# Optimization experiments

Hardware: AMD Instinct MI355X
Metric: run time of the kernel (lower is better)

Reference implementation:

```python
import jax, jax.numpy as jnp
import numpy as np

B, V, F, H, W = 8, 5023, 9976, 512, 512
L = 5  # lights


def setup_inputs() -> dict:
    key = jax.random.key(0)
    ks = jax.random.split(key, 7)
    return {
        "vertices": jax.random.normal(ks[0], (B, V, 3), jnp.float32),
        "transformed_vertices": jax.random.normal(ks[1], (B, V, 3), jnp.float32),
        "lights": jax.random.normal(ks[2], (B, L, 6), jnp.float32),
        "images": jax.random.uniform(ks[3], (B, 3, H, W), jnp.float32),
        "bary": jax.random.uniform(ks[4], (B, H, W, 3), jnp.float32) + 1e-3,
        "faces": jax.random.randint(ks[5], (F, 3), 0, V),
        "pix_to_face": jax.random.randint(ks[6], (B, H, W), 0, F + 1),  # ==F -> background
    }


def _face_vertices(verts, faces):
    # verts [B,V,3], faces [F,3] -> [B,F,3,3]  (gather)
    return verts[:, faces]


def _vertex_normals(verts, faces):
    # gather face verts, per-face cross products, scatter-add back to vertices
    fv = verts[:, faces]                       # [B,F,3,3]
    v0, v1, v2 = fv[:, :, 0], fv[:, :, 1], fv[:, :, 2]
    n = jnp.zeros_like(verts)
    n = n.at[:, faces[:, 1]].add(jnp.cross(v2 - v1, v0 - v1))
    n = n.at[:, faces[:, 2]].add(jnp.cross(v0 - v2, v1 - v2))
    n = n.at[:, faces[:, 0]].add(jnp.cross(v1 - v0, v2 - v0))
    return n / jnp.maximum(jnp.linalg.norm(n, axis=-1, keepdims=True), 1e-6)


def _add_directionlight(normals, lights):
    # normals [B,N,3], lights [B,L,6] -> shading [B,N,3]
    d = lights[:, :, :3]
    d = d / jnp.maximum(jnp.linalg.norm(d, axis=-1, keepdims=True), 1e-12)
    ndl = jnp.clip(jnp.einsum("bnc,blc->bln", normals, d), 0.0, 1.0)  # [B,L,N]
    return jnp.mean(ndl[..., None] * lights[:, :, None, 3:], axis=1)


def reference(vertices, transformed_vertices, lights, images, bary, faces, pix_to_face):
    sg = jax.lax.stop_gradient
    b, nv, _ = vertices.shape
    nf = faces.shape[0]
    h, w = pix_to_face.shape[1], pix_to_face.shape[2]

    tv = transformed_vertices.at[:, :, 2].add(10.0)

    fverts = _face_vertices(vertices, faces)                 # [B,F,3,3]
    normals = _vertex_normals(vertices, faces)               # [B,V,3]
    fnorm = _face_vertices(normals, faces)                   # [B,F,3,3]
    tnorm = _vertex_normals(tv, faces)
    tfnorm = _face_vertices(tnorm, faces)

    colors = jnp.full((b, nf, 3, 3), 180.0 / 255.0, vertices.dtype)  # face_colors buffer
    uv = jnp.zeros((b, nf, 3, 3), vertices.dtype)                    # face_uvcoords (unused downstream)
    # attribute channels: [0:3]=albedo [3:6]=tfnorm [6:9]=verts [9:12]=fnorm [12:15]=uv
    attrs = jnp.concatenate([colors, sg(tfnorm), sg(fverts), fnorm, uv], axis=-1)  # [B,F,3,15]

    # --- rasterizer interpolation stage ---
    p2f = pix_to_face.reshape(b, -1)                         # [B,HW]
    valid = (p2f < nf).astype(vertices.dtype)[..., None]     # [B,HW,1] alpha channel
    fidx = jnp.minimum(p2f, nf - 1)
    pa = jax.vmap(lambda a, i: a[i])(attrs, fidx)            # [B,HW,3,15]
    bw = bary.reshape(b, -1, 3)
    bw = bw / jnp.sum(bw, axis=-1, keepdims=True)
    interp = jnp.einsum("bpk,bpkc->bpc", bw, pa)             # [B,HW,15]

    albedo = interp[..., 0:3]
    tnormal_map = sg(interp[..., 3:6])
    pos_mask = (tnormal_map[..., 2:3] < 0.15).astype(vertices.dtype)
    normal_images = sg(interp[..., 9:12])
    alpha = sg(valid) * pos_mask                             # [B,HW,1]

    shading = _add_directionlight(normal_images, lights)     # [B,HW,3]
    shaded = albedo * shading

    imgs = images.transpose(0, 2, 3, 1).reshape(b, -1, 3)
    out = shaded * alpha + imgs * (1.0 - alpha)              # [B,HW,3]
    return out.reshape(b, h, w, 3).transpose(0, 3, 1, 2)     # [B,3,H,W]
```

## Files before the change

### kernel.cpp

```cpp
#include <hip/hip_runtime.h>

namespace {

constexpr int kB = 8;
constexpr int kV = 5023;
constexpr int kF = 9976;
constexpr int kH = 512;
constexpr int kW = 512;
constexpr int kL = 5;
constexpr int kHW = kH * kW;
constexpr int kQ = kHW / 4;
constexpr int kCap = 32;

__device__ __forceinline__ void cross3(float ax, float ay, float az,
                                       float bx, float by, float bz,
                                       float& cx, float& cy, float& cz) {
  cx = ay * bz - az * by;
  cy = az * bx - ax * bz;
  cz = ax * by - ay * bx;
}

__global__ void init_kernel(int* __restrict__ cnt,
                            const float* __restrict__ lights,
                            float* __restrict__ ldir) {
  int idx = blockIdx.x * blockDim.x + threadIdx.x;
  for (int i = idx; i < kV; i += gridDim.x * blockDim.x) cnt[i] = 0;
  if (idx < kB * kL) {
    float dx = lights[idx * 6 + 0];
    float dy = lights[idx * 6 + 1];
    float dz = lights[idx * 6 + 2];
    float inv = 1.0f / fmaxf(sqrtf(dx * dx + dy * dy + dz * dz), 1e-12f);
    ldir[idx * 6 + 0] = dx * inv;
    ldir[idx * 6 + 1] = dy * inv;
    ldir[idx * 6 + 2] = dz * inv;
    ldir[idx * 6 + 3] = lights[idx * 6 + 3];
    ldir[idx * 6 + 4] = lights[idx * 6 + 4];
    ldir[idx * 6 + 5] = lights[idx * 6 + 5];
  }
}

__global__ void prep_kernel(const float* __restrict__ verts,
                            const float* __restrict__ tverts,
                            const int* __restrict__ faces,
                            int* __restrict__ cnt,
                            int* __restrict__ adj,
                            float4* __restrict__ fn) {
  int idx = blockIdx.x * blockDim.x + threadIdx.x;
  if (idx < kF) {
    int f = idx;
#pragma unroll
    for (int c = 0; c < 3; ++c) {
      int v = faces[f * 3 + c];
      int slot = atomicAdd(&cnt[v], 1);
      if (slot < kCap) adj[v * kCap + slot] = f;
    }
    return;
  }
  idx -= kF;
  if (idx >= kB * kF) return;
  int b = idx / kF;
  int f = idx - b * kF;
  int i0 = faces[f * 3 + 0];
  int i1 = faces[f * 3 + 1];
  int i2 = faces[f * 3 + 2];

  float nx, ny, nz, tx, ty, tz;
  {
    const float* vb = verts + (size_t)b * kV * 3;
    float v0x = vb[i0 * 3 + 0], v0y = vb[i0 * 3 + 1], v0z = vb[i0 * 3 + 2];
    float v1x = vb[i1 * 3 + 0], v1y = vb[i1 * 3 + 1], v1z = vb[i1 * 3 + 2];
    float v2x = vb[i2 * 3 + 0], v2y = vb[i2 * 3 + 1], v2z = vb[i2 * 3 + 2];
    cross3(v1x - v0x, v1y - v0y, v1z - v0z, v2x - v0x, v2y - v0y, v2z - v0z,
           nx, ny, nz);
  }
  {
    const float* vb = tverts + (size_t)b * kV * 3;
    float v0x = vb[i0 * 3 + 0], v0y = vb[i0 * 3 + 1], v0z = vb[i0 * 3 + 2] + 10.0f;
    float v1x = vb[i1 * 3 + 0], v1y = vb[i1 * 3 + 1], v1z = vb[i1 * 3 + 2] + 10.0f;
    float v2x = vb[i2 * 3 + 0], v2y = vb[i2 * 3 + 1], v2z = vb[i2 * 3 + 2] + 10.0f;
    cross3(v1x - v0x, v1y - v0y, v1z - v0z, v2x - v0x, v2y - v0y, v2z - v0z,
           tx, ty, tz);
  }
  fn[(size_t)idx * 2 + 0] = make_float4(nx, ny, nz, tx);
  fn[(size_t)idx * 2 + 1] = make_float4(ty, tz, 0.0f, 0.0f);
}

__global__ void gather_normalize_kernel(const int* __restrict__ cnt,
                                        const int* __restrict__ adj,
                                        const float4* __restrict__ fn,
                                        float* __restrict__ normals,
                                        float* __restrict__ tz) {
  int idx = blockIdx.x * blockDim.x + threadIdx.x;
  if (idx >= kB * kV) return;
  int b = idx / kV;
  int v = idx - b * kV;
  int e = min(cnt[v], kCap);
  float nx = 0.f, ny = 0.f, nz = 0.f, tx = 0.f, ty = 0.f, tzv = 0.f;
  const int* av = adj + v * kCap;
  for (int j = 0; j < e; ++j) {
    int f = av[j];
    size_t k = ((size_t)b * kF + f) * 2;
    float4 a = fn[k];
    float4 c = fn[k + 1];
    nx += a.x;
    ny += a.y;
    nz += a.z;
    tx += a.w;
    ty += c.x;
    tzv += c.y;
  }
  float inv = 1.0f / fmaxf(sqrtf(nx * nx + ny * ny + nz * nz), 1e-6f);
  normals[(size_t)idx * 3 + 0] = nx * inv;
  normals[(size_t)idx * 3 + 1] = ny * inv;
  normals[(size_t)idx * 3 + 2] = nz * inv;
  float invt = 1.0f / fmaxf(sqrtf(tx * tx + ty * ty + tzv * tzv), 1e-6f);
  tz[idx] = tzv * invt;
}

__global__ void faceattr_kernel(const int* __restrict__ faces,
                                const float* __restrict__ normals,
                                const float* __restrict__ tz,
                                float4* __restrict__ fattr) {
  int idx = blockIdx.x * blockDim.x + threadIdx.x;
  if (idx >= kB * kF) return;
  int b = idx / kF;
  int f = idx - b * kF;
  int i0 = faces[f * 3 + 0];
  int i1 = faces[f * 3 + 1];
  int i2 = faces[f * 3 + 2];
  const float* nb = normals + (size_t)b * kV * 3;
  const float* tzb = tz + (size_t)b * kV;
  fattr[(size_t)idx * 3 + 0] =
      make_float4(nb[i0 * 3 + 0], nb[i0 * 3 + 1], nb[i0 * 3 + 2], tzb[i0]);
  fattr[(size_t)idx * 3 + 1] =
      make_float4(nb[i1 * 3 + 0], nb[i1 * 3 + 1], nb[i1 * 3 + 2], tzb[i1]);
  fattr[(size_t)idx * 3 + 2] =
      make_float4(nb[i2 * 3 + 0], nb[i2 * 3 + 1], nb[i2 * 3 + 2], tzb[i2]);
}

__global__ void __launch_bounds__(256) pixel4_kernel(
    const int4* __restrict__ p2f4,
    const float4* __restrict__ bary4,
    const float4* __restrict__ fattr,
    const float* __restrict__ ldir,
    const float4* __restrict__ img4,
    float4* __restrict__ out4) {
  int g = blockIdx.x * blockDim.x + threadIdx.x;
  if (g >= kB * kQ) return;
  int b = g / kQ;
  int q = g - b * kQ;

  int4 f4 = p2f4[g];
  float4 w0 = bary4[(size_t)g * 3 + 0];
  float4 w1 = bary4[(size_t)g * 3 + 1];
  float4 w2 = bary4[(size_t)g * 3 + 2];

  int fi[4] = {f4.x, f4.y, f4.z, f4.w};
  float bw[4][3] = {{w0.x, w0.y, w0.z},
                    {w0.w, w1.x, w1.y},
                    {w1.z, w1.w, w2.x},
                    {w2.y, w2.z, w2.w}};

  float4 a[4][3];
  bool valid[4];
#pragma unroll
  for (int k = 0; k < 4; ++k) {
    bool v = fi[k] < kF;
    valid[k] = v;
    int f = v ? fi[k] : (kF - 1);
    size_t base = ((size_t)b * kF + f) * 3;
    a[k][0] = fattr[base + 0];
    a[k][1] = fattr[base + 1];
    a[k][2] = fattr[base + 2];
  }

  size_t ibase = (size_t)b * 3 * kQ + q;
  float4 im0 = img4[ibase + 0 * (size_t)kQ];
  float4 im1 = img4[ibase + 1 * (size_t)kQ];
  float4 im2 = img4[ibase + 2 * (size_t)kQ];
  float im[3][4] = {{im0.x, im0.y, im0.z, im0.w},
                    {im1.x, im1.y, im1.z, im1.w},
                    {im2.x, im2.y, im2.z, im2.w}};

  const float* lb = ldir + (size_t)b * kL * 6;
  float lv[kL][6];
#pragma unroll
  for (int l = 0; l < kL; ++l)
#pragma unroll
    for (int c = 0; c < 6; ++c) lv[l][c] = lb[l * 6 + c];

  float o[3][4];
#pragma unroll
  for (int k = 0; k < 4; ++k) {
    float b0 = bw[k][0], b1 = bw[k][1], b2 = bw[k][2];
    float inv = 1.0f / (b0 + b1 + b2);
    b0 *= inv;
    b1 *= inv;
    b2 *= inv;
    float4 A = a[k][0], Bv = a[k][1], C = a[k][2];
    float tzi = b0 * A.w + b1 * Bv.w + b2 * C.w;
    bool alpha = valid[k] && (tzi < 0.15f);
    float nx = b0 * A.x + b1 * Bv.x + b2 * C.x;
    float ny = b0 * A.y + b1 * Bv.y + b2 * C.y;
    float nz = b0 * A.z + b1 * Bv.z + b2 * C.z;
    float s0 = 0.f, s1 = 0.f, s2 = 0.f;
#pragma unroll
    for (int l = 0; l < kL; ++l) {
      float d = nx * lv[l][0] + ny * lv[l][1] + nz * lv[l][2];
      d = fminf(fmaxf(d, 0.0f), 1.0f);
      s0 += d * lv[l][3];
      s1 += d * lv[l][4];
      s2 += d * lv[l][5];
    }
    const float kk = (180.0f / 255.0f) / (float)kL;
    o[0][k] = alpha ? kk * s0 : im[0][k];
    o[1][k] = alpha ? kk * s1 : im[1][k];
    o[2][k] = alpha ? kk * s2 : im[2][k];
  }

  out4[ibase + 0 * (size_t)kQ] = make_float4(o[0][0], o[0][1], o[0][2], o[0][3]);
  out4[ibase + 1 * (size_t)kQ] = make_float4(o[1][0], o[1][1], o[1][2], o[1][3]);
  out4[ibase + 2 * (size_t)kQ] = make_float4(o[2][0], o[2][1], o[2][2], o[2][3]);
}

}

extern "C" void kernel_launch(void* const* d_in, const int* in_sizes, int n_in,
                              void* d_out, int out_size, void* d_ws, size_t ws_size,
                              hipStream_t stream) {
  const float* vertices = (const float*)d_in[0];
  const float* tvertices = (const float*)d_in[1];
  const float* lights = (const float*)d_in[2];
  const float* images = (const float*)d_in[3];
  const float* bary = (const float*)d_in[4];
  const int* faces = (const int*)d_in[5];
  const int* p2f = (const int*)d_in[6];
  float* out = (float*)d_out;

  char* ws = (char*)d_ws;
  int* cnt = (int*)ws;
  ws += ((size_t)kV * sizeof(int) + 15) & ~15ull;
  int* adj = (int*)ws;
  ws += ((size_t)kV * kCap * sizeof(int) + 15) & ~15ull;
  float4* fn = (float4*)ws;
  ws += (size_t)kB * kF * 2 * sizeof(float4);
  float* normals = (float*)ws;
  ws += ((size_t)kB * kV * 3 * sizeof(float) + 15) & ~15ull;
  float* tz = (float*)ws;
  ws += ((size_t)kB * kV * sizeof(float) + 15) & ~15ull;
  float* ldir = (float*)ws;
  ws += ((size_t)kB * kL * 6 * sizeof(float) + 15) & ~15ull;
  float4* fattr = (float4*)ws;

  {
    init_kernel<<<20, 256, 0, stream>>>(cnt, lights, ldir);
  }
  {
    int n = kF + kB * kF;
    prep_kernel<<<(n + 255) / 256, 256, 0, stream>>>(vertices, tvertices, faces, cnt,
                                                     adj, fn);
  }
  {
    int n = kB * kV;
    gather_normalize_kernel<<<(n + 255) / 256, 256, 0, stream>>>(cnt, adj, fn, normals,
                                                                 tz);
  }
  {
    int n = kB * kF;
    faceattr_kernel<<<(n + 255) / 256, 256, 0, stream>>>(faces, normals, tz, fattr);
  }
  {
    int n = kB * kQ;
    pixel4_kernel<<<(n + 255) / 256, 256, 0, stream>>>((const int4*)p2f, (const float4*)bary,
                                                       fattr, ldir, (const float4*)images,
                                                       (float4*)out);
  }
}
```

Before: 57.17 us.

## Pack per-face normals as fp16 into 32-byte records and use nontemporal output stores

Each face's three vertex normals are stored as fp16, with the tz values kept in fp32, so a face record shrinks from 48 to 32 bytes and the pixel kernel's random gather fetches two 16-byte vectors instead of three. Light parameters are padded to float4, and their base index is made wave-uniform with readfirstlane so the loads can become scalar. Output stores use nontemporal hints to avoid polluting the cache. In exchange, normals lose precision in fp16, which slightly perturbs the shading values.

```diff
diff --git a/kernel.cpp b/kernel.cpp
--- a/kernel.cpp
+++ b/kernel.cpp
@@ -1,4 +1,5 @@
 #include <hip/hip_runtime.h>
+#include <stdint.h>
 
 namespace {
 
@@ -12,6 +13,21 @@
 constexpr int kQ = kHW / 4;
 constexpr int kCap = 32;
 
+typedef float nfloat4 __attribute__((ext_vector_type(4)));
+
+__device__ __forceinline__ float h2f(uint32_t u) {
+  _Float16 h;
+  uint16_t s = (uint16_t)u;
+  __builtin_memcpy(&h, &s, 2);
+  return (float)h;
+}
+__device__ __forceinline__ uint32_t f2h(float f) {
+  _Float16 h = (_Float16)f;
+  uint16_t s;
+  __builtin_memcpy(&s, &h, 2);
+  return (uint32_t)s;
+}
+
 __device__ __forceinline__ void cross3(float ax, float ay, float az,
                                        float bx, float by, float bz,
                                        float& cx, float& cy, float& cz) {
@@ -22,7 +38,7 @@
 
 __global__ void init_kernel(int* __restrict__ cnt,
                             const float* __restrict__ lights,
-                            float* __restrict__ ldir) {
+                            float4* __restrict__ ldir4) {
   int idx = blockIdx.x * blockDim.x + threadIdx.x;
   for (int i = idx; i < kV; i += gridDim.x * blockDim.x) cnt[i] = 0;
   if (idx < kB * kL) {
@@ -30,12 +46,9 @@
     float dy = lights[idx * 6 + 1];
     float dz = lights[idx * 6 + 2];
     float inv = 1.0f / fmaxf(sqrtf(dx * dx + dy * dy + dz * dz), 1e-12f);
-    ldir[idx * 6 + 0] = dx * inv;
-    ldir[idx * 6 + 1] = dy * inv;
-    ldir[idx * 6 + 2] = dz * inv;
-    ldir[idx * 6 + 3] = lights[idx * 6 + 3];
-    ldir[idx * 6 + 4] = lights[idx * 6 + 4];
-    ldir[idx * 6 + 5] = lights[idx * 6 + 5];
+    ldir4[idx * 2 + 0] = make_float4(dx * inv, dy * inv, dz * inv, 0.0f);
+    ldir4[idx * 2 + 1] =
+        make_float4(lights[idx * 6 + 3], lights[idx * 6 + 4], lights[idx * 6 + 5], 0.0f);
   }
 }
 
@@ -120,7 +133,7 @@
 __global__ void faceattr_kernel(const int* __restrict__ faces,
                                 const float* __restrict__ normals,
                                 const float* __restrict__ tz,
-                                float4* __restrict__ fattr) {
+                                uint4* __restrict__ fattr) {
   int idx = blockIdx.x * blockDim.x + threadIdx.x;
   if (idx >= kB * kF) return;
   int b = idx / kF;
@@ -130,19 +143,34 @@
   int i2 = faces[f * 3 + 2];
   const float* nb = normals + (size_t)b * kV * 3;
   const float* tzb = tz + (size_t)b * kV;
-  fattr[(size_t)idx * 3 + 0] =
-      make_float4(nb[i0 * 3 + 0], nb[i0 * 3 + 1], nb[i0 * 3 + 2], tzb[i0]);
-  fattr[(size_t)idx * 3 + 1] =
-      make_float4(nb[i1 * 3 + 0], nb[i1 * 3 + 1], nb[i1 * 3 + 2], tzb[i1]);
-  fattr[(size_t)idx * 3 + 2] =
-      make_float4(nb[i2 * 3 + 0], nb[i2 * 3 + 1], nb[i2 * 3 + 2], tzb[i2]);
+  uint32_t h[9];
+  h[0] = f2h(nb[i0 * 3 + 0]);
+  h[1] = f2h(nb[i0 * 3 + 1]);
+  h[2] = f2h(nb[i0 * 3 + 2]);
+  h[3] = f2h(nb[i1 * 3 + 0]);
+  h[4] = f2h(nb[i1 * 3 + 1]);
+  h[5] = f2h(nb[i1 * 3 + 2]);
+  h[6] = f2h(nb[i2 * 3 + 0]);
+  h[7] = f2h(nb[i2 * 3 + 1]);
+  h[8] = f2h(nb[i2 * 3 + 2]);
+  uint4 w0, w1;
+  w0.x = h[0] | (h[1] << 16);
+  w0.y = h[2] | (h[3] << 16);
+  w0.z = h[4] | (h[5] << 16);
+  w0.w = h[6] | (h[7] << 16);
+  w1.x = h[8];
+  w1.y = __float_as_uint(tzb[i0]);
+  w1.z = __float_as_uint(tzb[i1]);
+  w1.w = __float_as_uint(tzb[i2]);
+  fattr[(size_t)idx * 2 + 0] = w0;
+  fattr[(size_t)idx * 2 + 1] = w1;
 }
 
 __global__ void __launch_bounds__(256) pixel4_kernel(
     const int4* __restrict__ p2f4,
     const float4* __restrict__ bary4,
-    const float4* __restrict__ fattr,
-    const float* __restrict__ ldir,
+    const uint4* __restrict__ fattr,
+    const float4* __restrict__ ldir4,
     const float4* __restrict__ img4,
     float4* __restrict__ out4) {
   int g = blockIdx.x * blockDim.x + threadIdx.x;
@@ -161,17 +189,16 @@
                     {w1.z, w1.w, w2.x},
                     {w2.y, w2.z, w2.w}};
 
-  float4 a[4][3];
+  uint4 A[4], T[4];
   bool valid[4];
 #pragma unroll
   for (int k = 0; k < 4; ++k) {
     bool v = fi[k] < kF;
     valid[k] = v;
     int f = v ? fi[k] : (kF - 1);
-    size_t base = ((size_t)b * kF + f) * 3;
-    a[k][0] = fattr[base + 0];
-    a[k][1] = fattr[base + 1];
-    a[k][2] = fattr[base + 2];
+    size_t base = ((size_t)b * kF + f) * 2;
+    A[k] = fattr[base + 0];
+    T[k] = fattr[base + 1];
   }
 
   size_t ibase = (size_t)b * 3 * kQ + q;
@@ -182,12 +209,20 @@
                     {im1.x, im1.y, im1.z, im1.w},
                     {im2.x, im2.y, im2.z, im2.w}};
 
-  const float* lb = ldir + (size_t)b * kL * 6;
-  float lv[kL][6];
-#pragma unroll
-  for (int l = 0; l < kL; ++l)
-#pragma unroll
-    for (int c = 0; c < 6; ++c) lv[l][c] = lb[l * 6 + c];
+  int bu = __builtin_amdgcn_readfirstlane(b);
+  const float4* lb4 = ldir4 + (size_t)bu * kL * 2;
+  float ld[kL][3], lc[kL][3];
+#pragma unroll
+  for (int l = 0; l < kL; ++l) {
+    float4 d = lb4[l * 2 + 0];
+    float4 c = lb4[l * 2 + 1];
+    ld[l][0] = d.x;
+    ld[l][1] = d.y;
+    ld[l][2] = d.z;
+    lc[l][0] = c.x;
+    lc[l][1] = c.y;
+    lc[l][2] = c.z;
+  }
 
   float o[3][4];
 #pragma unroll
@@ -197,20 +232,28 @@
     b0 *= inv;
     b1 *= inv;
     b2 *= inv;
-    float4 A = a[k][0], Bv = a[k][1], C = a[k][2];
-    float tzi = b0 * A.w + b1 * Bv.w + b2 * C.w;
+    float n0x = h2f(A[k].x), n0y = h2f(A[k].x >> 16);
+    float n0z = h2f(A[k].y), n1x = h2f(A[k].y >> 16);
+    float n1y = h2f(A[k].z), n1z = h2f(A[k].z >> 16);
+    float n2x = h2f(A[k].w), n2y = h2f(A[k].w >> 16);
+    float n2z = h2f(T[k].x);
+    float tz0 = __uint_as_float(T[k].y);
+    float tz1 = __uint_as_float(T[k].z);
+    float tz2 = __uint_as_float(T[k].w);
+
+    float tzi = b0 * tz0 + b1 * tz1 + b2 * tz2;
     bool alpha = valid[k] && (tzi < 0.15f);
-    float nx = b0 * A.x + b1 * Bv.x + b2 * C.x;
-    float ny = b0 * A.y + b1 * Bv.y + b2 * C.y;
-    float nz = b0 * A.z + b1 * Bv.z + b2 * C.z;
+    float nx = b0 * n0x + b1 * n1x + b2 * n2x;
+    float ny = b0 * n0y + b1 * n1y + b2 * n2y;
+    float nz = b0 * n0z + b1 * n1z + b2 * n2z;
     float s0 = 0.f, s1 = 0.f, s2 = 0.f;
 #pragma unroll
     for (int l = 0; l < kL; ++l) {
-      float d = nx * lv[l][0] + ny * lv[l][1] + nz * lv[l][2];
+      float d = nx * ld[l][0] + ny * ld[l][1] + nz * ld[l][2];
       d = fminf(fmaxf(d, 0.0f), 1.0f);
-      s0 += d * lv[l][3];
-      s1 += d * lv[l][4];
-      s2 += d * lv[l][5];
+      s0 += d * lc[l][0];
+      s1 += d * lc[l][1];
+      s2 += d * lc[l][2];
     }
     const float kk = (180.0f / 255.0f) / (float)kL;
     o[0][k] = alpha ? kk * s0 : im[0][k];
@@ -218,9 +261,11 @@
     o[2][k] = alpha ? kk * s2 : im[2][k];
   }
 
-  out4[ibase + 0 * (size_t)kQ] = make_float4(o[0][0], o[0][1], o[0][2], o[0][3]);
-  out4[ibase + 1 * (size_t)kQ] = make_float4(o[1][0], o[1][1], o[1][2], o[1][3]);
-  out4[ibase + 2 * (size_t)kQ] = make_float4(o[2][0], o[2][1], o[2][2], o[2][3]);
+#pragma unroll
+  for (int c = 0; c < 3; ++c) {
+    nfloat4 v = {o[c][0], o[c][1], o[c][2], o[c][3]};
+    __builtin_nontemporal_store(v, (nfloat4*)&out4[ibase + c * (size_t)kQ]);
+  }
 }
 
 }
@@ -248,12 +293,12 @@
   ws += ((size_t)kB * kV * 3 * sizeof(float) + 15) & ~15ull;
   float* tz = (float*)ws;
   ws += ((size_t)kB * kV * sizeof(float) + 15) & ~15ull;
-  float* ldir = (float*)ws;
-  ws += ((size_t)kB * kL * 6 * sizeof(float) + 15) & ~15ull;
-  float4* fattr = (float4*)ws;
-
-  {
-    init_kernel<<<20, 256, 0, stream>>>(cnt, lights, ldir);
+  float4* ldir4 = (float4*)ws;
+  ws += (size_t)kB * kL * 2 * sizeof(float4);
+  uint4* fattr = (uint4*)ws;
+
+  {
+    init_kernel<<<20, 256, 0, stream>>>(cnt, lights, ldir4);
   }
   {
     int n = kF + kB * kF;
@@ -272,7 +317,7 @@
   {
     int n = kB * kQ;
     pixel4_kernel<<<(n + 255) / 256, 256, 0, stream>>>((const int4*)p2f, (const float4*)bary,
-                                                       fattr, ldir, (const float4*)images,
+                                                       fattr, ldir4, (const float4*)images,
                                                        (float4*)out);
   }
 }
```

Result: faster. 50.64 us (-11.4%).
